# Kernel optimization log

Hardware: AMD Instinct MI355X
Metric: run time of the kernel (lower is better)

The kernel has to match this reference:

```python
import jax, jax.numpy as jnp
import numpy as np

N_HEAD = 12
HEAD_DIM = 64
EPS = 1e-6
ROPE_BASE = 10000.0


def rms_norm(x, w):
    x32 = x.astype(jnp.float32)
    var = jnp.mean(x32 * x32, axis=-1, keepdims=True)
    xn = x32 * jax.lax.rsqrt(var + EPS)
    return w * xn.astype(x.dtype)


def rotate_half(x):
    x1, x2 = jnp.split(x, 2, axis=-1)
    return jnp.concatenate((-x2, x1), axis=-1)


def rope_cos_sin(seq_len, dtype):
    inv_freq = 1.0 / (ROPE_BASE ** (jnp.arange(0, HEAD_DIM, 2, dtype=jnp.float32) / HEAD_DIM))
    pos = jnp.arange(seq_len, dtype=jnp.float32)
    freqs = pos[:, None] * inv_freq[None, :]          # [S, HEAD_DIM//2]
    emb = jnp.concatenate((freqs, freqs), axis=-1)    # [S, HEAD_DIM]
    # shape [1, 1, S, HEAD_DIM] (batch, head, seq, dim) after unsqueeze_dim=1
    return emb[None, None].astype(dtype), None  # placeholder, see below


def setup_inputs() -> dict:
    key = jax.random.key(0)
    ks = jax.random.split(key, 9)
    B, S, D, F = 1, 4096, 768, 2048
    s = 0.02
    return {
        "hidden_states": jax.random.normal(ks[0], (B, S, D), jnp.float32),
        "w_q": jax.random.normal(ks[1], (D, D), jnp.float32) * s,
        "w_k": jax.random.normal(ks[2], (D, D), jnp.float32) * s,
        "w_v": jax.random.normal(ks[3], (D, D), jnp.float32) * s,
        "w_o": jax.random.normal(ks[4], (D, D), jnp.float32) * s,
        "w_gate": jax.random.normal(ks[5], (D, F), jnp.float32) * s,
        "w_up": jax.random.normal(ks[6], (D, F), jnp.float32) * s,
        "w_down": jax.random.normal(ks[7], (F, D), jnp.float32) * s,
        "w_norm1": jnp.ones((D,), jnp.float32),
        "w_norm2": jnp.ones((D,), jnp.float32),
    }


def attention(x, w_q, w_k, w_v, w_o):
    B, S, D = x.shape
    scale = HEAD_DIM ** -0.5
    # project and split heads: [B, H, S, hd]
    q = (x @ w_q).reshape(B, S, N_HEAD, HEAD_DIM).transpose(0, 2, 1, 3)
    k = (x @ w_k).reshape(B, S, N_HEAD, HEAD_DIM).transpose(0, 2, 1, 3)
    v = (x @ w_v).reshape(B, S, N_HEAD, HEAD_DIM).transpose(0, 2, 1, 3)
    # rotary embedding (position_ids = arange(S))
    inv_freq = 1.0 / (ROPE_BASE ** (jnp.arange(0, HEAD_DIM, 2, dtype=jnp.float32) / HEAD_DIM))
    pos = jnp.arange(S, dtype=jnp.float32)
    freqs = pos[:, None] * inv_freq[None, :]
    emb = jnp.concatenate((freqs, freqs), axis=-1)          # [S, hd]
    cos = jnp.cos(emb).astype(x.dtype)[None, None]          # [1,1,S,hd]
    sin = jnp.sin(emb).astype(x.dtype)[None, None]
    q = q * cos + rotate_half(q) * sin
    k = k * cos + rotate_half(k) * sin
    # eager attention with causal mask (materialized, as in the original)
    scores = jnp.einsum("bhqd,bhkd->bhqk", q, k) * scale
    causal = jnp.triu(jnp.ones((S, S), dtype=bool), k=1)
    scores = jnp.where(causal, jnp.finfo(scores.dtype).min, scores)
    attn = jax.nn.softmax(scores.astype(jnp.float32), axis=-1).astype(q.dtype)
    out = jnp.einsum("bhqk,bhkd->bhqd", attn, v)
    out = out.transpose(0, 2, 1, 3).reshape(B, S, D)
    return out @ w_o


def reference(hidden_states, w_q, w_k, w_v, w_o, w_gate, w_up, w_down, w_norm1, w_norm2):
    x = hidden_states
    h = x + attention(rms_norm(x, w_norm1), w_q, w_k, w_v, w_o)
    y = rms_norm(h, w_norm2)
    ffn = (jax.nn.silu(y @ w_gate) * (y @ w_up)) @ w_down
    return h + ffn
```

## Files before the change

kernel.cpp:

```cpp
#include <hip/hip_runtime.h>
#include <hip/hip_bf16.h>

typedef __attribute__((ext_vector_type(8))) short s8v;
typedef __attribute__((ext_vector_type(4))) float f4v;
typedef __attribute__((ext_vector_type(16))) float f16v;
typedef __attribute__((ext_vector_type(4))) unsigned u4v;

typedef __attribute__((address_space(1))) const void as1_void;
typedef __attribute__((address_space(3))) void as3_void;

__device__ __forceinline__ void gl16(const void* g, void* l) {
  __builtin_amdgcn_global_load_lds((as1_void*)g, (as3_void*)l, 16, 0, 0);
}

__device__ __forceinline__ float b2f(int u) {
  union { float f; unsigned i; } c; c.i = ((unsigned)(u & 0xFFFF)) << 16; return c.f;
}
__device__ __forceinline__ unsigned short f2b(float f) {
  union { float f; unsigned i; } c; c.f = f;
  unsigned r = c.i + 0x7FFFu + ((c.i >> 16) & 1u);
  return (unsigned short)(r >> 16);
}
__device__ __forceinline__ unsigned pk2(float lo, float hi) {
  unsigned u;
  asm("v_cvt_pk_bf16_f32 %0, %1, %2" : "=v"(u) : "v"(lo), "v"(hi));
  return u;
}

#define MFMA16(a, b, c) __builtin_amdgcn_mfma_f32_16x16x32_bf16((a), (b), (c), 0, 0, 0)
#define MFMA32(a, b, c) __builtin_amdgcn_mfma_f32_32x32x16_bf16((a), (b), (c), 0, 0, 0)

struct Seg { const float* src; unsigned short* dst; int K; int N; int nbn; int nblocks; int mode; };
struct PrepArgs { Seg seg[8]; float* ct; float* st; };

__global__ __launch_bounds__(256) void prep_k(PrepArgs a) {
  int b = blockIdx.x, si = 0;
  while (si < 7 && b >= a.seg[si].nblocks) { b -= a.seg[si].nblocks; ++si; }
  const Seg s = a.seg[si];
  const int tid = threadIdx.x;
  if (s.mode == 3) {
    const int t = b * 256 + tid;
    const int sq = t >> 5, d = t & 31;
    const float inv = powf(10000.0f, -(float)d * (1.0f / 32.0f));
    const float ang = (float)sq * inv;
    a.ct[t] = cosf(ang);
    a.st[t] = sinf(ang);
    return;
  }
  __shared__ float tile[32][33];
  const int tx = tid & 31, ty = tid >> 5;
  const int bn = b % s.nbn, bk = b / s.nbn;
#pragma unroll
  for (int i = 0; i < 32; i += 8)
    tile[ty + i][tx] = s.src[(size_t)(bk * 32 + ty + i) * s.N + bn * 32 + tx];
  __syncthreads();
#pragma unroll
  for (int i = 0; i < 32; i += 8) {
    int row;
    if (s.mode == 0)      row = bn * 32 + ty + i;
    else                  row = bn * 64 + (s.mode == 2 ? 32 : 0) + ty + i;
    s.dst[(size_t)row * s.K + bk * 32 + tx] = f2b(tile[tx][ty + i]);
  }
}

__global__ __launch_bounds__(256) void rmsnorm_k(const float* __restrict__ x,
    const float* __restrict__ w, unsigned short* __restrict__ out) {
  const int row = blockIdx.x, tid = threadIdx.x;
  const float* xr = x + (size_t)row * 768;
  float v0 = xr[tid], v1 = xr[tid + 256], v2 = xr[tid + 512];
  float ss = v0 * v0 + v1 * v1 + v2 * v2;
#pragma unroll
  for (int m = 1; m < 64; m <<= 1) ss += __shfl_xor(ss, m, 64);
  __shared__ float sred[4];
  if ((tid & 63) == 0) sred[tid >> 6] = ss;
  __syncthreads();
  const float tot = sred[0] + sred[1] + sred[2] + sred[3];
  const float rn = rsqrtf(tot * (1.0f / 768.0f) + 1e-6f);
  unsigned short* orow = out + (size_t)row * 768;
  orow[tid]       = f2b(v0 * rn * w[tid]);
  orow[tid + 256] = f2b(v1 * rn * w[tid + 256]);
  orow[tid + 512] = f2b(v2 * rn * w[tid + 512]);
}

template <int EPI, int BN>
__global__ __launch_bounds__(256) void gemm_bt(const unsigned short* __restrict__ A,
    const unsigned short* __restrict__ Bt, unsigned short* __restrict__ Cb,
    float* __restrict__ Cf, const float* __restrict__ R, int K, int ldc,
    const float* __restrict__ ct, const float* __restrict__ st) {
  constexpr int ABYTES = 128 * 32 * 2;
  constexpr int BBYTES = BN * 32 * 2;
  constexpr int MR = (BN == 128) ? 4 : 2;
  __shared__ unsigned short As[3 * 128 * 32];
  __shared__ unsigned short Bs[3 * BN * 32];
  const int tid = threadIdx.x;
  const int lane = tid & 63, wid = tid >> 6;
  const int wrow = (BN == 128) ? (wid >> 1) * 64 : wid * 32;
  const int wcol = (BN == 128) ? (wid & 1) * 64 : 0;
  const int l15 = lane & 15, l4 = lane >> 4;
  const int bm = blockIdx.y, bn = blockIdx.x;

  f4v acc[MR][4] = {};

  const int o0 = tid * 16, o1 = tid * 16 + 4096;
  const int r0 = o0 >> 6, c0 = o0 & 63;
  const int r1 = o1 >> 6, c1 = o1 & 63;
  const size_t ldab = (size_t)K * 2;
  const char* Abyte = (const char*)A;
  const char* Bbyte = (const char*)Bt;
  const size_t a0 = (size_t)(bm * 128 + r0) * ldab + c0;
  const size_t a1 = (size_t)(bm * 128 + r1) * ldab + c1;
  const size_t b0 = (size_t)(bn * BN + r0) * ldab + c0;
  const size_t b1 = (size_t)(bn * BN + r1) * ldab + c1;
  char* AsB = (char*)As;
  char* BsB = (char*)Bs;
  const int uoff = wid << 10;

#define STAGEK(I, SL) do { const size_t kb = (size_t)(I) * 64;                 \
    char* Aw = AsB + (SL) * ABYTES;                                            \
    char* Bw = BsB + (SL) * BBYTES;                                            \
    gl16(Abyte + a0 + kb, Aw + uoff);                                          \
    gl16(Abyte + a1 + kb, Aw + uoff + 4096);                                   \
    gl16(Bbyte + b0 + kb, Bw + uoff);                                          \
    if constexpr (BN == 128) gl16(Bbyte + b1 + kb, Bw + uoff + 4096); } while (0)

  const int NI = K >> 5;
  STAGEK(0, 0);
  STAGEK(1, 1);
  int sel = 0, nsl = 2;

  for (int i = 0; i < NI; ++i) {
    if (i < NI - 1) {
      if constexpr (BN == 128) asm volatile("s_waitcnt vmcnt(4)" ::: "memory");
      else                     asm volatile("s_waitcnt vmcnt(3)" ::: "memory");
    } else {
      asm volatile("s_waitcnt vmcnt(0)" ::: "memory");
    }
    __builtin_amdgcn_s_barrier();
    __builtin_amdgcn_sched_barrier(0);
    if (i + 2 < NI) STAGEK(i + 2, nsl);
    const char* Ar = AsB + sel * ABYTES;
    const char* Br = BsB + sel * BBYTES;
    s8v af[MR], bf[4];
#pragma unroll
    for (int m = 0; m < MR; ++m)
      af[m] = *(const s8v*)(Ar + (wrow + m * 16 + l15) * 64 + l4 * 16);
#pragma unroll
    for (int n = 0; n < 4; ++n)
      bf[n] = *(const s8v*)(Br + (wcol + n * 16 + l15) * 64 + l4 * 16);
    __builtin_amdgcn_s_setprio(1);
#pragma unroll
    for (int m = 0; m < MR; ++m)
#pragma unroll
      for (int n = 0; n < 4; ++n) acc[m][n] = MFMA16(af[m], bf[n], acc[m][n]);
    __builtin_amdgcn_s_setprio(0);
    sel = (sel == 2) ? 0 : sel + 1;
    nsl = (nsl == 2) ? 0 : nsl + 1;
  }
#undef STAGEK

  const int row0 = bm * 128 + wrow;
  const int col0 = bn * BN + wcol;

  if (EPI == 2 && bn < 12) {
#pragma unroll
    for (int m = 0; m < MR; ++m)
#pragma unroll
      for (int r = 0; r < 4; ++r) {
        const int row = row0 + m * 16 + l4 * 4 + r;
#pragma unroll
        for (int n = 0; n < 2; ++n) {
          const int d = n * 16 + l15;
          const float c  = ct[row * 32 + d];
          const float sn = st[row * 32 + d];
          const float aa = acc[m][n][r], bb = acc[m][n + 2][r];
          acc[m][n][r]     = aa * c - bb * sn;
          acc[m][n + 2][r] = bb * c + aa * sn;
        }
      }
  }

  if (EPI == 3) {
    const int wcx = wcol >> 6;
    const int colb = (bn * 2 + wcx) * 32;
#pragma unroll
    for (int m = 0; m < MR; ++m)
#pragma unroll
      for (int n = 0; n < 2; ++n)
#pragma unroll
        for (int r = 0; r < 4; ++r) {
          const int row = row0 + m * 16 + l4 * 4 + r;
          const float g = acc[m][n][r], u = acc[m][n + 2][r];
          const float val = g * u / (1.0f + __expf(-g));
          Cb[(size_t)row * 2048 + colb + n * 16 + l15] = f2b(val);
        }
    return;
  }

#pragma unroll
  for (int m = 0; m < MR; ++m)
#pragma unroll
    for (int n = 0; n < 4; ++n)
#pragma unroll
      for (int r = 0; r < 4; ++r) {
        const int row = row0 + m * 16 + l4 * 4 + r;
        const int col = col0 + n * 16 + l15;
        const float v = acc[m][n][r];
        if (EPI == 1) {
          Cf[(size_t)row * ldc + col] = v + R[(size_t)row * ldc + col];
        } else {
          Cb[(size_t)row * ldc + col] = f2b(v);
        }
      }
}

__global__ __launch_bounds__(256, 3) void flash_k(const unsigned short* __restrict__ qkv,
    float4* __restrict__ Opart, float2* __restrict__ ml) {
  const int kh = blockIdx.x, p = blockIdx.y, h = blockIdx.z;
  const int qbA = 63 - p;
  const int tid = threadIdx.x;
  const int wv = tid >> 6, lane = tid & 63;
  const int l31 = lane & 31, h8 = lane >> 5;
  const int myqb = (wv & 1) ? p : qbA;
  const int qrel = (wv >> 1) * 32 + l31;
  const int q_abs = myqb * 64 + qrel;

  __shared__ unsigned short Ks[2][64 * 72];
  __shared__ unsigned short Vt[2][64 * 72];

  const unsigned short* qp = qkv + h * 64;
  const unsigned short* kp = qkv + 768 + h * 64;
  const unsigned short* vp = qkv + 1536 + h * 64;

  s8v qf[4];
#pragma unroll
  for (int c = 0; c < 4; ++c)
    qf[c] = *(const s8v*)(qp + (size_t)q_abs * 2304 + c * 16 + h8 * 8);

  f16v o0 = {}, o1 = {};
  float m_s = -1e30f, l_s = 0.f;

  const int krow = tid >> 3, kc = (tid & 7) * 8;
  const int vj = tid & 31, vd0 = (tid >> 5) * 8;

  s8v ka, kb, va, vb;
#define LOADT(T) do { const size_t k0n = (size_t)(T) * 64;                    \
    ka = *(const s8v*)(kp + (k0n + krow) * 2304 + kc);                        \
    kb = *(const s8v*)(kp + (k0n + krow + 32) * 2304 + kc);                   \
    va = *(const s8v*)(vp + (k0n + 2 * vj) * 2304 + vd0);                     \
    vb = *(const s8v*)(vp + (k0n + 2 * vj + 1) * 2304 + vd0); } while (0)
#define WRITET(BUF) do {                                                      \
    *(s8v*)(Ks[BUF] + krow * 72 + kc) = ka;                                   \
    *(s8v*)(Ks[BUF] + (krow + 32) * 72 + kc) = kb;                            \
    unsigned* vtw = (unsigned*)(Vt[BUF] + (size_t)vd0 * 72 + 2 * vj);         \
    _Pragma("unroll")                                                         \
    for (int i = 0; i < 8; ++i)                                               \
      vtw[i * 36] = ((unsigned)(unsigned short)va[i]) |                       \
                    (((unsigned)(unsigned short)vb[i]) << 16); } while (0)

  LOADT(kh);
  WRITET(0);
  if (kh + 2 <= qbA) LOADT(kh + 2);
  __syncthreads();

  for (int t = kh; t <= qbA; t += 2) {
    const int cur = (t >> 1) & 1;
    if (t <= myqb) {
      f16v s0 = {}, s1 = {};
      __builtin_amdgcn_s_setprio(1);
#pragma unroll
      for (int c = 0; c < 4; ++c) {
        const s8v kf0 = *(const s8v*)(Ks[cur] + l31 * 72 + c * 16 + h8 * 8);
        const s8v kf1 = *(const s8v*)(Ks[cur] + (32 + l31) * 72 + c * 16 + h8 * 8);
        s0 = MFMA32(kf0, qf[c], s0);
        s1 = MFMA32(kf1, qf[c], s1);
      }
      __builtin_amdgcn_s_setprio(0);
#pragma unroll
      for (int r = 0; r < 16; ++r) { s0[r] *= 0.125f; s1[r] *= 0.125f; }
      if (t == myqb) {
#pragma unroll
        for (int r = 0; r < 16; ++r) {
          const int koff = (r & 3) + 8 * (r >> 2) + 4 * h8;
          if (koff > qrel) s0[r] = -1e30f;
          if (koff + 32 > qrel) s1[r] = -1e30f;
        }
      }
      float red[8];
#pragma unroll
      for (int i = 0; i < 8; ++i)
        red[i] = fmaxf(fmaxf(s0[i], s0[i + 8]), fmaxf(s1[i], s1[i + 8]));
#pragma unroll
      for (int i = 0; i < 4; ++i) red[i] = fmaxf(red[i], red[i + 4]);
      float mloc = fmaxf(fmaxf(red[0], red[1]), fmaxf(red[2], red[3]));
      mloc = fmaxf(mloc, __shfl_xor(mloc, 32));
      if (__any(mloc > m_s + 8.f)) {
        const float mn = fmaxf(m_s, mloc);
        const float corr = __expf(m_s - mn);
        m_s = mn; l_s *= corr;
#pragma unroll
        for (int r = 0; r < 16; ++r) { o0[r] *= corr; o1[r] *= corr; }
      }
#pragma unroll
      for (int r = 0; r < 16; ++r) {
        s0[r] = __expf(s0[r] - m_s);
        s1[r] = __expf(s1[r] - m_s);
      }
      float sm[8];
#pragma unroll
      for (int i = 0; i < 8; ++i) sm[i] = (s0[i] + s0[i + 8]) + (s1[i] + s1[i + 8]);
#pragma unroll
      for (int i = 0; i < 4; ++i) sm[i] += sm[i + 4];
      float ps = (sm[0] + sm[1]) + (sm[2] + sm[3]);
      ps += __shfl_xor(ps, 32);
      l_s += ps;

      unsigned pk0[8], pk1[8];
#pragma unroll
      for (int g = 0; g < 4; ++g)
#pragma unroll
        for (int j = 0; j < 2; ++j) {
          pk0[g * 2 + j] = pk2(s0[g * 4 + 2 * j], s0[g * 4 + 2 * j + 1]);
          pk1[g * 2 + j] = pk2(s1[g * 4 + 2 * j], s1[g * 4 + 2 * j + 1]);
        }
      __builtin_amdgcn_s_setprio(1);
#pragma unroll
      for (int c = 0; c < 4; ++c) {
        const int g0 = (c & 1) * 2, g1 = g0 + 1;
        const unsigned pA0 = (c & 2) ? pk1[g0 * 2 + 0] : pk0[g0 * 2 + 0];
        const unsigned pA1 = (c & 2) ? pk1[g0 * 2 + 1] : pk0[g0 * 2 + 1];
        const unsigned pB0 = (c & 2) ? pk1[g1 * 2 + 0] : pk0[g1 * 2 + 0];
        const unsigned pB1 = (c & 2) ? pk1[g1 * 2 + 1] : pk0[g1 * 2 + 1];
        const unsigned t00 = __shfl_xor((int)pA0, 32);
        const unsigned t01 = __shfl_xor((int)pA1, 32);
        const unsigned t10 = __shfl_xor((int)pB0, 32);
        const unsigned t11 = __shfl_xor((int)pB1, 32);
        union { u4v u; s8v s; } pf;
        pf.u[0] = h8 ? t10 : pA0;
        pf.u[1] = h8 ? t11 : pA1;
        pf.u[2] = h8 ? pB0 : t00;
        pf.u[3] = h8 ? pB1 : t01;
        const s8v vf0 = *(const s8v*)(Vt[cur] + l31 * 72 + c * 16 + h8 * 8);
        const s8v vf1 = *(const s8v*)(Vt[cur] + (32 + l31) * 72 + c * 16 + h8 * 8);
        o0 = MFMA32(vf0, pf.s, o0);
        o1 = MFMA32(vf1, pf.s, o1);
      }
      __builtin_amdgcn_s_setprio(0);
    }
    if (t + 2 <= qbA) {
      WRITET(cur ^ 1);
      if (t + 4 <= qbA) LOADT(t + 4);
      __syncthreads();
    }
  }

  const size_t obase = (size_t)kh * 12 * 16 * 4096;
#pragma unroll
  for (int g = 0; g < 4; ++g) {
    const float4 v0 = make_float4(o0[g * 4], o0[g * 4 + 1], o0[g * 4 + 2], o0[g * 4 + 3]);
    const float4 v1 = make_float4(o1[g * 4], o1[g * 4 + 1], o1[g * 4 + 2], o1[g * 4 + 3]);
    const int dg0 = 2 * g + h8;
    const int dg1 = 8 + 2 * g + h8;
    Opart[obase + ((size_t)h * 16 + dg0) * 4096 + q_abs] = v0;
    Opart[obase + ((size_t)h * 16 + dg1) * 4096 + q_abs] = v1;
  }
  if (h8 == 0)
    ml[(size_t)kh * 12 * 4096 + (size_t)h * 4096 + q_abs] = make_float2(m_s, l_s);
#undef LOADT
#undef WRITET
}

__global__ __launch_bounds__(256) void combine_k(const float4* __restrict__ Opart,
    const float2* __restrict__ ml, unsigned short* __restrict__ out) {
  const int u = blockIdx.x * 256 + threadIdx.x;
  const int q = u & 4095;
  const int rest = u >> 12;
  const int dgrp = rest & 15;
  const int h = rest >> 4;
  const float2 e0 = ml[h * 4096 + q];
  const float2 e1 = ml[12 * 4096 + h * 4096 + q];
  const float mx = fmaxf(e0.x, e1.x);
  const float w0 = __expf(e0.x - mx), w1 = __expf(e1.x - mx);
  const float inv = 1.0f / (w0 * e0.y + w1 * e1.y);
  const size_t idx = ((size_t)h * 16 + dgrp) * 4096 + q;
  const float4 a = Opart[idx];
  const float4 b = Opart[(size_t)12 * 16 * 4096 + idx];
  const int dbase = (dgrp < 8) ? 4 * dgrp : 32 + 4 * (dgrp - 8);
  ushort4 r;
  r.x = f2b((w0 * a.x + w1 * b.x) * inv);
  r.y = f2b((w0 * a.y + w1 * b.y) * inv);
  r.z = f2b((w0 * a.z + w1 * b.z) * inv);
  r.w = f2b((w0 * a.w + w1 * b.w) * inv);
  *(ushort4*)(out + (size_t)q * 768 + h * 64 + dbase) = r;
}

extern "C" void kernel_launch(void* const* d_in, const int* in_sizes, int n_in,
                              void* d_out, int out_size, void* d_ws, size_t ws_size,
                              hipStream_t stream) {
  const float* x    = (const float*)d_in[0];
  const float* w_q  = (const float*)d_in[1];
  const float* w_k  = (const float*)d_in[2];
  const float* w_v  = (const float*)d_in[3];
  const float* w_o  = (const float*)d_in[4];
  const float* w_g  = (const float*)d_in[5];
  const float* w_u  = (const float*)d_in[6];
  const float* w_d  = (const float*)d_in[7];
  const float* w_n1 = (const float*)d_in[8];
  const float* w_n2 = (const float*)d_in[9];
  (void)in_sizes; (void)n_in; (void)out_size; (void)ws_size;

  char* ws = (char*)d_ws;
  size_t off = 0;
  auto alloc = [&](size_t bytes) { char* p = ws + off; off += (bytes + 255) & ~(size_t)255; return p; };
  unsigned short* wqkvT = (unsigned short*)alloc(2304ull * 768 * 2);
  unsigned short* woT   = (unsigned short*)alloc(768ull * 768 * 2);
  unsigned short* wguT  = (unsigned short*)alloc(4096ull * 768 * 2);
  unsigned short* wdT   = (unsigned short*)alloc(768ull * 2048 * 2);
  float* ct             = (float*)alloc(4096ull * 32 * 4);
  float* st             = (float*)alloc(4096ull * 32 * 4);
  unsigned short* xn    = (unsigned short*)alloc(4096ull * 768 * 2);
  unsigned short* qkv   = (unsigned short*)alloc(4096ull * 2304 * 2);
  unsigned short* attn  = (unsigned short*)alloc(4096ull * 768 * 2);
  float* hbuf           = (float*)alloc(4096ull * 768 * 4);
  unsigned short* ybuf  = (unsigned short*)alloc(4096ull * 768 * 2);
  unsigned short* ffn   = (unsigned short*)alloc(4096ull * 2048 * 2);
  float4* Opart         = (float4*)alloc(2ull * 12 * 16 * 4096 * 16);
  float2* mlb           = (float2*)alloc(2ull * 12 * 4096 * 8);

  PrepArgs pa;
  pa.seg[0] = { w_q, wqkvT,                 768,  768, 24,  576, 0 };
  pa.seg[1] = { w_k, wqkvT + 768 * 768,     768,  768, 24,  576, 0 };
  pa.seg[2] = { w_v, wqkvT + 2 * 768 * 768, 768,  768, 24,  576, 0 };
  pa.seg[3] = { w_o, woT,                   768,  768, 24,  576, 0 };
  pa.seg[4] = { w_g, wguT,                  768, 2048, 64, 1536, 1 };
  pa.seg[5] = { w_u, wguT,                  768, 2048, 64, 1536, 2 };
  pa.seg[6] = { w_d, wdT,                  2048,  768, 24, 1536, 0 };
  pa.seg[7] = { nullptr, nullptr, 0, 0, 0, 512, 3 };
  pa.ct = ct; pa.st = st;
  const int prep_blocks = 576 * 4 + 1536 * 3 + 512;

  prep_k<<<prep_blocks, 256, 0, stream>>>(pa);
  rmsnorm_k<<<4096, 256, 0, stream>>>(x, w_n1, xn);
  gemm_bt<2, 128><<<dim3(18, 32), 256, 0, stream>>>(xn, wqkvT, qkv, nullptr, nullptr, 768, 2304, ct, st);
  flash_k<<<dim3(2, 32, 12), 256, 0, stream>>>(qkv, Opart, mlb);
  combine_k<<<3072, 256, 0, stream>>>(Opart, mlb, attn);
  gemm_bt<1, 64><<<dim3(12, 32), 256, 0, stream>>>(attn, woT, nullptr, hbuf, x, 768, 768, nullptr, nullptr);
  rmsnorm_k<<<4096, 256, 0, stream>>>(hbuf, w_n2, ybuf);
  gemm_bt<3, 128><<<dim3(32, 32), 256, 0, stream>>>(ybuf, wguT, ffn, nullptr, nullptr, 768, 2048, nullptr, nullptr);
  gemm_bt<1, 64><<<dim3(12, 32), 256, 0, stream>>>(ffn, wdT, nullptr, (float*)d_out, hbuf, 2048, 768, nullptr, nullptr);
}
```

Measured before the change: 225.4 us.

## Fuse first RMSNorm into prep, fold softmax scale into Q, remap flash blocks

Folds the first RMSNorm into the prep kernel as an extra segment, which removes one kernel launch. The attention scale and log2(e) are folded into the Q projection epilogue, so the flash kernel can use exp2f directly and skip a per-score multiply. The online-softmax max reduction now uses v_max3 and a wider rescale threshold. The flash grid is flattened to one dimension with a custom mapping that interleaves long and short causal blocks across heads to balance load. The wider threshold risks larger intermediate exponent ranges, and the prep kernel grows larger.

```diff
diff --git a/kernel.cpp b/kernel.cpp
--- a/kernel.cpp
+++ b/kernel.cpp
@@ -26,16 +26,21 @@
   asm("v_cvt_pk_bf16_f32 %0, %1, %2" : "=v"(u) : "v"(lo), "v"(hi));
   return u;
 }
+__device__ __forceinline__ float max3f(float a, float b, float c) {
+  float d;
+  asm("v_max3_f32 %0, %1, %2, %3" : "=v"(d) : "v"(a), "v"(b), "v"(c));
+  return d;
+}
 
 #define MFMA16(a, b, c) __builtin_amdgcn_mfma_f32_16x16x32_bf16((a), (b), (c), 0, 0, 0)
 #define MFMA32(a, b, c) __builtin_amdgcn_mfma_f32_32x32x16_bf16((a), (b), (c), 0, 0, 0)
 
 struct Seg { const float* src; unsigned short* dst; int K; int N; int nbn; int nblocks; int mode; };
-struct PrepArgs { Seg seg[8]; float* ct; float* st; };
+struct PrepArgs { Seg seg[9]; float* ct; float* st; const float* wn1; };
 
 __global__ __launch_bounds__(256) void prep_k(PrepArgs a) {
   int b = blockIdx.x, si = 0;
-  while (si < 7 && b >= a.seg[si].nblocks) { b -= a.seg[si].nblocks; ++si; }
+  while (si < 8 && b >= a.seg[si].nblocks) { b -= a.seg[si].nblocks; ++si; }
   const Seg s = a.seg[si];
   const int tid = threadIdx.x;
   if (s.mode == 3) {
@@ -45,6 +50,23 @@
     const float ang = (float)sq * inv;
     a.ct[t] = cosf(ang);
     a.st[t] = sinf(ang);
+    return;
+  }
+  if (s.mode == 4) {
+    const float* xr = s.src + (size_t)b * 768;
+    float v0 = xr[tid], v1 = xr[tid + 256], v2 = xr[tid + 512];
+    float ss = v0 * v0 + v1 * v1 + v2 * v2;
+#pragma unroll
+    for (int m = 1; m < 64; m <<= 1) ss += __shfl_xor(ss, m, 64);
+    __shared__ float sred[4];
+    if ((tid & 63) == 0) sred[tid >> 6] = ss;
+    __syncthreads();
+    const float tot = sred[0] + sred[1] + sred[2] + sred[3];
+    const float rn = rsqrtf(tot * (1.0f / 768.0f) + 1e-6f);
+    unsigned short* orow = s.dst + (size_t)b * 768;
+    orow[tid]       = f2b(v0 * rn * a.wn1[tid]);
+    orow[tid + 256] = f2b(v1 * rn * a.wn1[tid + 256]);
+    orow[tid + 512] = f2b(v2 * rn * a.wn1[tid + 512]);
     return;
   }
   __shared__ float tile[32][33];
@@ -178,6 +200,15 @@
         }
       }
   }
+  if (EPI == 2 && bn < 6) {
+    const float QSC = 0.18033688011112042f;
+#pragma unroll
+    for (int m = 0; m < MR; ++m)
+#pragma unroll
+      for (int n = 0; n < 4; ++n)
+#pragma unroll
+        for (int r = 0; r < 4; ++r) acc[m][n][r] *= QSC;
+  }
 
   if (EPI == 3) {
     const int wcx = wcol >> 6;
@@ -215,7 +246,14 @@
 
 __global__ __launch_bounds__(256, 3) void flash_k(const unsigned short* __restrict__ qkv,
     float4* __restrict__ Opart, float2* __restrict__ ml) {
-  const int kh = blockIdx.x, p = blockIdx.y, h = blockIdx.z;
+  const int b = blockIdx.x;
+  const int c = b & 255, r = b >> 8;
+  const int w = c >> 5, v = c & 31;
+  int p, s;
+  if (r == 0)      { p = v;                 s = w; }
+  else if (r == 1) { p = 31 - v;            s = w + 8; }
+  else             { p = 4 * w + (v >> 3);  s = 16 + (v & 7); }
+  const int kh = s & 1, h = s >> 1;
   const int qbA = 63 - p;
   const int tid = threadIdx.x;
   const int wv = tid >> 6, lane = tid & 63;
@@ -233,8 +271,8 @@
 
   s8v qf[4];
 #pragma unroll
-  for (int c = 0; c < 4; ++c)
-    qf[c] = *(const s8v*)(qp + (size_t)q_abs * 2304 + c * 16 + h8 * 8);
+  for (int cc = 0; cc < 4; ++cc)
+    qf[cc] = *(const s8v*)(qp + (size_t)q_abs * 2304 + cc * 16 + h8 * 8);
 
   f16v o0 = {}, o1 = {};
   float m_s = -1e30f, l_s = 0.f;
@@ -268,42 +306,38 @@
       f16v s0 = {}, s1 = {};
       __builtin_amdgcn_s_setprio(1);
 #pragma unroll
-      for (int c = 0; c < 4; ++c) {
-        const s8v kf0 = *(const s8v*)(Ks[cur] + l31 * 72 + c * 16 + h8 * 8);
-        const s8v kf1 = *(const s8v*)(Ks[cur] + (32 + l31) * 72 + c * 16 + h8 * 8);
-        s0 = MFMA32(kf0, qf[c], s0);
-        s1 = MFMA32(kf1, qf[c], s1);
+      for (int cc = 0; cc < 4; ++cc) {
+        const s8v kf0 = *(const s8v*)(Ks[cur] + l31 * 72 + cc * 16 + h8 * 8);
+        const s8v kf1 = *(const s8v*)(Ks[cur] + (32 + l31) * 72 + cc * 16 + h8 * 8);
+        s0 = MFMA32(kf0, qf[cc], s0);
+        s1 = MFMA32(kf1, qf[cc], s1);
       }
       __builtin_amdgcn_s_setprio(0);
-#pragma unroll
-      for (int r = 0; r < 16; ++r) { s0[r] *= 0.125f; s1[r] *= 0.125f; }
       if (t == myqb) {
 #pragma unroll
-        for (int r = 0; r < 16; ++r) {
-          const int koff = (r & 3) + 8 * (r >> 2) + 4 * h8;
-          if (koff > qrel) s0[r] = -1e30f;
-          if (koff + 32 > qrel) s1[r] = -1e30f;
+        for (int rr = 0; rr < 16; ++rr) {
+          const int koff = (rr & 3) + 8 * (rr >> 2) + 4 * h8;
+          if (koff > qrel) s0[rr] = -1e30f;
+          if (koff + 32 > qrel) s1[rr] = -1e30f;
         }
       }
-      float red[8];
+      float u[8];
 #pragma unroll
       for (int i = 0; i < 8; ++i)
-        red[i] = fmaxf(fmaxf(s0[i], s0[i + 8]), fmaxf(s1[i], s1[i + 8]));
-#pragma unroll
-      for (int i = 0; i < 4; ++i) red[i] = fmaxf(red[i], red[i + 4]);
-      float mloc = fmaxf(fmaxf(red[0], red[1]), fmaxf(red[2], red[3]));
+        u[i] = fmaxf(max3f(s0[i], s0[i + 8], s1[i]), s1[i + 8]);
+      float mloc = fmaxf(max3f(max3f(max3f(u[0], u[1], u[2]), u[3], u[4]), u[5], u[6]), u[7]);
       mloc = fmaxf(mloc, __shfl_xor(mloc, 32));
-      if (__any(mloc > m_s + 8.f)) {
+      if (__any(mloc > m_s + 11.0f)) {
         const float mn = fmaxf(m_s, mloc);
-        const float corr = __expf(m_s - mn);
+        const float corr = exp2f(m_s - mn);
         m_s = mn; l_s *= corr;
 #pragma unroll
-        for (int r = 0; r < 16; ++r) { o0[r] *= corr; o1[r] *= corr; }
-      }
-#pragma unroll
-      for (int r = 0; r < 16; ++r) {
-        s0[r] = __expf(s0[r] - m_s);
-        s1[r] = __expf(s1[r] - m_s);
+        for (int rr = 0; rr < 16; ++rr) { o0[rr] *= corr; o1[rr] *= corr; }
+      }
+#pragma unroll
+      for (int rr = 0; rr < 16; ++rr) {
+        s0[rr] = exp2f(s0[rr] - m_s);
+        s1[rr] = exp2f(s1[rr] - m_s);
       }
       float sm[8];
 #pragma unroll
@@ -324,12 +358,12 @@
         }
       __builtin_amdgcn_s_setprio(1);
 #pragma unroll
-      for (int c = 0; c < 4; ++c) {
-        const int g0 = (c & 1) * 2, g1 = g0 + 1;
-        const unsigned pA0 = (c & 2) ? pk1[g0 * 2 + 0] : pk0[g0 * 2 + 0];
-        const unsigned pA1 = (c & 2) ? pk1[g0 * 2 + 1] : pk0[g0 * 2 + 1];
-        const unsigned pB0 = (c & 2) ? pk1[g1 * 2 + 0] : pk0[g1 * 2 + 0];
-        const unsigned pB1 = (c & 2) ? pk1[g1 * 2 + 1] : pk0[g1 * 2 + 1];
+      for (int cc = 0; cc < 4; ++cc) {
+        const int g0 = (cc & 1) * 2, g1 = g0 + 1;
+        const unsigned pA0 = (cc & 2) ? pk1[g0 * 2 + 0] : pk0[g0 * 2 + 0];
+        const unsigned pA1 = (cc & 2) ? pk1[g0 * 2 + 1] : pk0[g0 * 2 + 1];
+        const unsigned pB0 = (cc & 2) ? pk1[g1 * 2 + 0] : pk0[g1 * 2 + 0];
+        const unsigned pB1 = (cc & 2) ? pk1[g1 * 2 + 1] : pk0[g1 * 2 + 1];
         const unsigned t00 = __shfl_xor((int)pA0, 32);
         const unsigned t01 = __shfl_xor((int)pA1, 32);
         const unsigned t10 = __shfl_xor((int)pB0, 32);
@@ -339,8 +373,8 @@
         pf.u[1] = h8 ? t11 : pA1;
         pf.u[2] = h8 ? pB0 : t00;
         pf.u[3] = h8 ? pB1 : t01;
-        const s8v vf0 = *(const s8v*)(Vt[cur] + l31 * 72 + c * 16 + h8 * 8);
-        const s8v vf1 = *(const s8v*)(Vt[cur] + (32 + l31) * 72 + c * 16 + h8 * 8);
+        const s8v vf0 = *(const s8v*)(Vt[cur] + l31 * 72 + cc * 16 + h8 * 8);
+        const s8v vf1 = *(const s8v*)(Vt[cur] + (32 + l31) * 72 + cc * 16 + h8 * 8);
         o0 = MFMA32(vf0, pf.s, o0);
         o1 = MFMA32(vf1, pf.s, o1);
       }
@@ -379,7 +413,7 @@
   const float2 e0 = ml[h * 4096 + q];
   const float2 e1 = ml[12 * 4096 + h * 4096 + q];
   const float mx = fmaxf(e0.x, e1.x);
-  const float w0 = __expf(e0.x - mx), w1 = __expf(e1.x - mx);
+  const float w0 = exp2f(e0.x - mx), w1 = exp2f(e1.x - mx);
   const float inv = 1.0f / (w0 * e0.y + w1 * e1.y);
   const size_t idx = ((size_t)h * 16 + dgrp) * 4096 + q;
   const float4 a = Opart[idx];
@@ -435,13 +469,13 @@
   pa.seg[5] = { w_u, wguT,                  768, 2048, 64, 1536, 2 };
   pa.seg[6] = { w_d, wdT,                  2048,  768, 24, 1536, 0 };
   pa.seg[7] = { nullptr, nullptr, 0, 0, 0, 512, 3 };
-  pa.ct = ct; pa.st = st;
-  const int prep_blocks = 576 * 4 + 1536 * 3 + 512;
+  pa.seg[8] = { x, xn, 0, 0, 0, 4096, 4 };
+  pa.ct = ct; pa.st = st; pa.wn1 = w_n1;
+  const int prep_blocks = 576 * 4 + 1536 * 3 + 512 + 4096;
 
   prep_k<<<prep_blocks, 256, 0, stream>>>(pa);
-  rmsnorm_k<<<4096, 256, 0, stream>>>(x, w_n1, xn);
   gemm_bt<2, 128><<<dim3(18, 32), 256, 0, stream>>>(xn, wqkvT, qkv, nullptr, nullptr, 768, 2304, ct, st);
-  flash_k<<<dim3(2, 32, 12), 256, 0, stream>>>(qkv, Opart, mlb);
+  flash_k<<<768, 256, 0, stream>>>(qkv, Opart, mlb);
   combine_k<<<3072, 256, 0, stream>>>(Opart, mlb, attn);
   gemm_bt<1, 64><<<dim3(12, 32), 256, 0, stream>>>(attn, woT, nullptr, hbuf, x, 768, 768, nullptr, nullptr);
   rmsnorm_k<<<4096, 256, 0, stream>>>(hbuf, w_n2, ybuf);
```

New measurement: 236.6 us. 5.0% more time.
